# Optimization experiments

Hardware: AMD Instinct MI355X
Metric: run time of the kernel (lower is better)

Reference implementation:

```python
import jax, jax.numpy as jnp
import numpy as np

N, E, IN, HID, OUT = 100000, 1600000, 128, 128, 64


def setup_inputs() -> dict:
    key = jax.random.key(0)
    ks = jax.random.split(key, 8)
    x = jax.random.normal(ks[0], (N, IN), dtype=jnp.float32)
    edge_index = jax.random.randint(ks[1], (2, E), 0, N, dtype=jnp.int64)
    s = lambda fan_in: 1.0 / np.sqrt(fan_in)
    W1_l = jax.random.normal(ks[2], (IN, HID), dtype=jnp.float32) * s(IN)
    W1_r = jax.random.normal(ks[3], (IN, HID), dtype=jnp.float32) * s(IN)
    b1 = jnp.zeros((HID,), dtype=jnp.float32)
    W2_l = jax.random.normal(ks[4], (HID, OUT), dtype=jnp.float32) * s(HID)
    W2_r = jax.random.normal(ks[5], (HID, OUT), dtype=jnp.float32) * s(HID)
    b2 = jnp.zeros((OUT,), dtype=jnp.float32)
    return {"x": x, "edge_index": edge_index, "W1_l": W1_l, "W1_r": W1_r,
            "b1": b1, "W2_l": W2_l, "W2_r": W2_r, "b2": b2}


def sage_conv(x, src, dst, W_l, W_r, b):
    """PyG SAGEConv (aggr='mean', root_weight=True): lin_l(mean_agg) + lin_r(x)."""
    n = x.shape[0]
    msg = x[src]                                              # [E, d] gather
    agg = jax.ops.segment_sum(msg, dst, num_segments=n)       # [N, d] scatter-add
    deg = jax.ops.segment_sum(jnp.ones_like(dst, dtype=x.dtype), dst,
                              num_segments=n)                 # [N]
    mean = agg / jnp.maximum(deg, 1.0)[:, None]
    return mean @ W_l + x @ W_r + b


def reference(x, edge_index, W1_l, W1_r, b1, W2_l, W2_r, b2):
    src, dst = edge_index[0], edge_index[1]
    h = sage_conv(x, src, dst, W1_l, W1_r, b1)
    h = jax.nn.relu(h)
    # dropout(p=0.5) is identity in eval mode
    out = sage_conv(h, src, dst, W2_l, W2_r, b2)
    return out
```

## Files before the change

### kernel.cpp

```cpp
#include <hip/hip_runtime.h>

#define NN 100000
#define NE 1600000
#define PSHIFT 9
#define PSZ 512
#define NP ((NN + PSZ - 1) / PSZ)
#define BCHUNK 8192
#define NBIN ((NE + BCHUNK - 1) / BCHUNK)
#define SRCMASK 0x1FFFF

typedef __attribute__((ext_vector_type(8))) short short8;
typedef __attribute__((ext_vector_type(4))) float f32x4;

__device__ __forceinline__ ushort f2bf(float f) {
    uint u = __float_as_uint(f);
    return (ushort)((u + 0x7FFFu + ((u >> 16) & 1u)) >> 16);
}
__device__ __forceinline__ float bflo(uint u) { return __uint_as_float(u << 16); }
__device__ __forceinline__ float bfhi(uint u) { return __uint_as_float(u & 0xffff0000u); }
__device__ __forceinline__ uint packbf(float a, float b) {
    return (uint)f2bf(a) | ((uint)f2bf(b) << 16);
}

__global__ __launch_bounds__(256) void k_phist(const int* __restrict__ dst,
                                               int* __restrict__ pcnt)
{
    __shared__ int cnt[256];
    const int tid = threadIdx.x;
    cnt[tid] = 0;
    __syncthreads();
    const long e0 = (long)blockIdx.x * BCHUNK;
    for (int i = tid; i < BCHUNK; i += 256) {
        long e = e0 + i;
        if (e < NE) atomicAdd(&cnt[dst[e] >> PSHIFT], 1);
    }
    __syncthreads();
    if (cnt[tid] > 0) atomicAdd(&pcnt[tid], cnt[tid]);
}

__global__ __launch_bounds__(256) void k_pscan(const int* __restrict__ pcnt,
                                               int* __restrict__ poff,
                                               int* __restrict__ gcur,
                                               int* __restrict__ rowptr)
{
    __shared__ int tmp[256];
    const int tid = threadIdx.x;
    int v = (tid < NP) ? pcnt[tid] : 0;
    tmp[tid] = v;
    __syncthreads();
    for (int off = 1; off < 256; off <<= 1) {
        int t = (tid >= off) ? tmp[tid - off] : 0;
        __syncthreads();
        tmp[tid] += t;
        __syncthreads();
    }
    int ex = tmp[tid] - v;
    if (tid < NP) { poff[tid] = ex; gcur[tid] = ex; }
    if (tid == 0) { poff[NP] = NE; rowptr[NN] = NE; }
}

__global__ __launch_bounds__(256) void k_binning(const int* __restrict__ src,
                                                 const int* __restrict__ dst,
                                                 int* __restrict__ gcur,
                                                 uint* __restrict__ packed)
{
    __shared__ int cnt[256];
    __shared__ int base[256];
    const int tid = threadIdx.x;
    const long e0 = (long)blockIdx.x * BCHUNK;
    cnt[tid] = 0;
    __syncthreads();
    for (int i = tid; i < BCHUNK; i += 256) {
        long e = e0 + i;
        if (e < NE) atomicAdd(&cnt[dst[e] >> PSHIFT], 1);
    }
    __syncthreads();
    if (cnt[tid] > 0) base[tid] = atomicAdd(&gcur[tid], cnt[tid]);
    cnt[tid] = 0;
    __syncthreads();
    for (int i = tid; i < BCHUNK; i += 256) {
        long e = e0 + i;
        if (e < NE) {
            int d = dst[e], s = src[e];
            int p = d >> PSHIFT;
            int ofs = atomicAdd(&cnt[p], 1);
            packed[base[p] + ofs] = (uint)s | ((uint)(d & (PSZ - 1)) << 17);
        }
    }
}

__global__ __launch_bounds__(256) void k_pfill(const uint* __restrict__ packed,
                                               const int* __restrict__ poff,
                                               int* __restrict__ rowptr,
                                               int* __restrict__ col)
{
    __shared__ int cnt[PSZ];
    __shared__ int cur[PSZ];
    __shared__ int tot[256];
    const int p   = blockIdx.x;
    const int tid = threadIdx.x;
    const int beg = poff[p], end = poff[p + 1];
    cnt[tid] = 0; cnt[tid + 256] = 0;
    __syncthreads();
    for (int i = beg + tid; i < end; i += 256)
        atomicAdd(&cnt[packed[i] >> 17], 1);
    __syncthreads();
    int v0 = cnt[tid * 2], v1 = cnt[tid * 2 + 1];
    int s  = v0 + v1;
    tot[tid] = s;
    __syncthreads();
    for (int off = 1; off < 256; off <<= 1) {
        int t = (tid >= off) ? tot[tid - off] : 0;
        __syncthreads();
        tot[tid] += t;
        __syncthreads();
    }
    int ex = tot[tid] - s + beg;
    cur[tid * 2]     = ex;
    cur[tid * 2 + 1] = ex + v0;
    int n0 = p * PSZ;
    if (n0 + tid * 2     < NN) rowptr[n0 + tid * 2]     = ex;
    if (n0 + tid * 2 + 1 < NN) rowptr[n0 + tid * 2 + 1] = ex + v0;
    __syncthreads();
    for (int i = beg + tid; i < end; i += 256) {
        uint v = packed[i];
        int pos = atomicAdd(&cur[v >> 17], 1);
        col[pos] = (int)(v & SRCMASK);
    }
}

__global__ __launch_bounds__(256) void k_castw(const float* __restrict__ W1l,
                                               const float* __restrict__ W1r,
                                               const float* __restrict__ W2l,
                                               const float* __restrict__ W2r,
                                               ushort* __restrict__ WbT1,
                                               ushort* __restrict__ WbT2)
{
    int i = blockIdx.x * 256 + threadIdx.x;
    if (i < 256 * 128) {
        int c = i >> 7, k = i & 127;
        float v = (c < 128) ? W1l[k * 128 + c] : W1r[k * 128 + (c - 128)];
        WbT1[i] = f2bf(v);
    } else if (i < 256 * 128 + 128 * 128) {
        int j = i - 256 * 128;
        int c = j >> 7, k = j & 127;
        float v = (c < 64) ? W2l[k * 64 + c] : W2r[k * 64 + (c - 64)];
        WbT2[j] = f2bf(v);
    }
}

template <bool IS_L1>
__global__ __launch_bounds__(256) void k_gemmf(const void* __restrict__ Ap,
                                               const ushort* __restrict__ Bt,
                                               const float* __restrict__ bias,
                                               ushort* __restrict__ zb,
                                               void* __restrict__ yout)
{
    constexpr int CB = IS_L1 ? 4 : 2;
    constexpr int ZW = IS_L1 ? 128 : 64;
    __shared__ ushort As[64 * 128];

    const int tid = threadIdx.x, bm = blockIdx.x;

    for (int c = tid; c < 1024; c += 256) {
        int row  = c >> 4;
        int coff = (c & 15) * 8;
        int gr   = bm * 64 + row;
        short8 va;
        if (gr < NN) {
            if (IS_L1) {
                const float* A = (const float*)Ap;
                float4 f0 = *reinterpret_cast<const float4*>(A + (size_t)gr * 128 + coff);
                float4 f1 = *reinterpret_cast<const float4*>(A + (size_t)gr * 128 + coff + 4);
                va[0] = (short)f2bf(f0.x); va[1] = (short)f2bf(f0.y);
                va[2] = (short)f2bf(f0.z); va[3] = (short)f2bf(f0.w);
                va[4] = (short)f2bf(f1.x); va[5] = (short)f2bf(f1.y);
                va[6] = (short)f2bf(f1.z); va[7] = (short)f2bf(f1.w);
            } else {
                const ushort* A = (const ushort*)Ap;
                va = *reinterpret_cast<const short8*>(A + (size_t)gr * 128 + coff);
            }
        } else {
            va = short8{0, 0, 0, 0, 0, 0, 0, 0};
        }
        int byte = row * 256 + coff * 2;
        byte ^= ((row & 7) << 4);
        *reinterpret_cast<short8*>(reinterpret_cast<char*>(As) + byte) = va;
    }
    __syncthreads();

    const int wid = tid >> 6, lane = tid & 63;
    const int lr  = lane & 15;
    const int lk  = (lane >> 4) << 3;

    f32x4 acc[4][CB];
#pragma unroll
    for (int mi = 0; mi < 4; ++mi)
#pragma unroll
        for (int nf = 0; nf < CB; ++nf) acc[mi][nf] = f32x4{0.f, 0.f, 0.f, 0.f};

    const char* pA = reinterpret_cast<const char*>(As);

#pragma unroll
    for (int ks = 0; ks < 4; ++ks) {
        int k2 = (ks * 32 + lk) * 2;
        short8 a[4], b[CB];
#pragma unroll
        for (int mi = 0; mi < 4; ++mi) {
            int r = mi * 16 + lr;
            int byte = r * 256 + k2;
            byte ^= ((r & 7) << 4);
            a[mi] = *reinterpret_cast<const short8*>(pA + byte);
        }
#pragma unroll
        for (int nf = 0; nf < CB; ++nf) {
            int colB = wid * (16 * CB) + nf * 16 + lr;
            b[nf] = *reinterpret_cast<const short8*>(Bt + (size_t)colB * 128 + ks * 32 + lk);
        }
#pragma unroll
        for (int mi = 0; mi < 4; ++mi)
#pragma unroll
            for (int nf = 0; nf < CB; ++nf)
                acc[mi][nf] = __builtin_amdgcn_mfma_f32_16x16x32_bf16(a[mi], b[nf], acc[mi][nf], 0, 0, 0);
    }

#pragma unroll
    for (int mi = 0; mi < 4; ++mi) {
#pragma unroll
        for (int nf = 0; nf < CB; ++nf) {
            int colg = wid * (16 * CB) + nf * 16 + lr;
#pragma unroll
            for (int rr = 0; rr < 4; ++rr) {
                int rowg = bm * 64 + mi * 16 + ((lane >> 4) << 2) + rr;
                if (rowg < NN) {
                    float v = acc[mi][nf][rr];
                    if (colg < ZW) {
                        zb[(size_t)rowg * ZW + colg] = f2bf(v);
                    } else {
                        int c2 = colg - ZW;
                        if (IS_L1) ((ushort*)yout)[(size_t)rowg * 128 + c2] = f2bf(v + bias[c2]);
                        else       ((float*)yout)[(size_t)rowg * 64 + c2]  = v + bias[c2];
                    }
                }
            }
        }
    }
}

__global__ __launch_bounds__(256) void k_gather1(const ushort* __restrict__ z1b,
                                                 const ushort* __restrict__ y1b,
                                                 const int* __restrict__ rowptr,
                                                 const int* __restrict__ col,
                                                 ushort* __restrict__ hb)
{
    const int w = threadIdx.x >> 6, lane = threadIdx.x & 63;
    const int n = blockIdx.x * 4 + w;
    if (n >= NN) return;
    const int half = lane >> 5, li = lane & 31;
    const int beg = rowptr[n], end = rowptr[n + 1];
    const uint2* zu = (const uint2*)z1b;
    float a0 = 0.f, a1 = 0.f, a2 = 0.f, a3 = 0.f;
    int e = beg;
    for (; e + 7 < end; e += 8) {
        int s0 = col[e     + half];
        int s1 = col[e + 2 + half];
        int s2 = col[e + 4 + half];
        int s3 = col[e + 6 + half];
        uint2 u0 = zu[(size_t)s0 * 32 + li];
        uint2 u1 = zu[(size_t)s1 * 32 + li];
        uint2 u2 = zu[(size_t)s2 * 32 + li];
        uint2 u3 = zu[(size_t)s3 * 32 + li];
        a0 += bflo(u0.x) + bflo(u1.x) + bflo(u2.x) + bflo(u3.x);
        a1 += bfhi(u0.x) + bfhi(u1.x) + bfhi(u2.x) + bfhi(u3.x);
        a2 += bflo(u0.y) + bflo(u1.y) + bflo(u2.y) + bflo(u3.y);
        a3 += bfhi(u0.y) + bfhi(u1.y) + bfhi(u2.y) + bfhi(u3.y);
    }
    for (; e + 1 < end; e += 2) {
        int s0 = col[e + half];
        uint2 u0 = zu[(size_t)s0 * 32 + li];
        a0 += bflo(u0.x); a1 += bfhi(u0.x);
        a2 += bflo(u0.y); a3 += bfhi(u0.y);
    }
    if (e < end && half == 0) {
        int s0 = col[e];
        uint2 u0 = zu[(size_t)s0 * 32 + li];
        a0 += bflo(u0.x); a1 += bfhi(u0.x);
        a2 += bflo(u0.y); a3 += bfhi(u0.y);
    }
    a0 += __shfl_xor(a0, 32); a1 += __shfl_xor(a1, 32);
    a2 += __shfl_xor(a2, 32); a3 += __shfl_xor(a3, 32);
    if (half == 0) {
        float inv = 1.0f / (float)max(end - beg, 1);
        uint2 uy = ((const uint2*)y1b)[(size_t)n * 32 + li];
        float h0 = fmaxf(a0 * inv + bflo(uy.x), 0.f);
        float h1 = fmaxf(a1 * inv + bfhi(uy.x), 0.f);
        float h2 = fmaxf(a2 * inv + bflo(uy.y), 0.f);
        float h3 = fmaxf(a3 * inv + bfhi(uy.y), 0.f);
        uint2 o;
        o.x = packbf(h0, h1);
        o.y = packbf(h2, h3);
        ((uint2*)hb)[(size_t)n * 32 + li] = o;
    }
}

__global__ __launch_bounds__(256) void k_gather2(const ushort* __restrict__ z2b,
                                                 const float* __restrict__ y2f,
                                                 const int* __restrict__ rowptr,
                                                 const int* __restrict__ col,
                                                 float* __restrict__ out)
{
    const int w = threadIdx.x >> 6, lane = threadIdx.x & 63;
    const int n = blockIdx.x * 4 + w;
    if (n >= NN) return;
    const int quar = lane >> 4, li = lane & 15;
    const int beg = rowptr[n], end = rowptr[n + 1];
    const uint2* zu = (const uint2*)z2b;
    float a0 = 0.f, a1 = 0.f, a2 = 0.f, a3 = 0.f;
    int e = beg;
    for (; e + 15 < end; e += 16) {
        int s0 = col[e      + quar];
        int s1 = col[e + 4  + quar];
        int s2 = col[e + 8  + quar];
        int s3 = col[e + 12 + quar];
        uint2 u0 = zu[(size_t)s0 * 16 + li];
        uint2 u1 = zu[(size_t)s1 * 16 + li];
        uint2 u2 = zu[(size_t)s2 * 16 + li];
        uint2 u3 = zu[(size_t)s3 * 16 + li];
        a0 += bflo(u0.x) + bflo(u1.x) + bflo(u2.x) + bflo(u3.x);
        a1 += bfhi(u0.x) + bfhi(u1.x) + bfhi(u2.x) + bfhi(u3.x);
        a2 += bflo(u0.y) + bflo(u1.y) + bflo(u2.y) + bflo(u3.y);
        a3 += bfhi(u0.y) + bfhi(u1.y) + bfhi(u2.y) + bfhi(u3.y);
    }
    for (; e + 3 < end; e += 4) {
        int s0 = col[e + quar];
        uint2 u0 = zu[(size_t)s0 * 16 + li];
        a0 += bflo(u0.x); a1 += bfhi(u0.x);
        a2 += bflo(u0.y); a3 += bfhi(u0.y);
    }
    int rem = end - e;
    if (quar < rem) {
        int s0 = col[e + quar];
        uint2 u0 = zu[(size_t)s0 * 16 + li];
        a0 += bflo(u0.x); a1 += bfhi(u0.x);
        a2 += bflo(u0.y); a3 += bfhi(u0.y);
    }
    a0 += __shfl_xor(a0, 16); a1 += __shfl_xor(a1, 16);
    a2 += __shfl_xor(a2, 16); a3 += __shfl_xor(a3, 16);
    a0 += __shfl_xor(a0, 32); a1 += __shfl_xor(a1, 32);
    a2 += __shfl_xor(a2, 32); a3 += __shfl_xor(a3, 32);
    if (quar == 0) {
        float inv = 1.0f / (float)max(end - beg, 1);
        float4 y = ((const float4*)y2f)[(size_t)n * 16 + li];
        float4 o;
        o.x = a0 * inv + y.x;
        o.y = a1 * inv + y.y;
        o.z = a2 * inv + y.z;
        o.w = a3 * inv + y.w;
        ((float4*)out)[(size_t)n * 16 + li] = o;
    }
}

extern "C" void kernel_launch(void* const* d_in, const int* in_sizes, int n_in,
                              void* d_out, int out_size, void* d_ws, size_t ws_size,
                              hipStream_t stream)
{
    const float* x   = (const float*)d_in[0];
    const int*   ei  = (const int*)d_in[1];
    const float* W1l = (const float*)d_in[2];
    const float* W1r = (const float*)d_in[3];
    const float* b1  = (const float*)d_in[4];
    const float* W2l = (const float*)d_in[5];
    const float* W2r = (const float*)d_in[6];
    const float* b2  = (const float*)d_in[7];
    float* out = (float*)d_out;

    const int* src = ei;
    const int* dst = ei + NE;

    int*  rowptr = (int*)d_ws;
    int*  pcnt   = rowptr + NN + 1;
    int*  poff   = pcnt + 256;
    int*  gcur   = poff + 256;
    uint* packed = (uint*)(gcur + 256);
    int*  colA   = (int*)(packed + NE);
    uintptr_t p = (uintptr_t)(colA + NE);
    p = (p + 255) & ~(uintptr_t)255;
    ushort* WbT1 = (ushort*)p;  p += (size_t)256 * 128 * 2;
    ushort* WbT2 = (ushort*)p;  p += (size_t)128 * 128 * 2;
    p = (p + 255) & ~(uintptr_t)255;
    ushort* z1b = (ushort*)p;   p += (size_t)NN * 128 * 2;
    ushort* y1b = (ushort*)p;   p += (size_t)NN * 128 * 2;
    ushort* hb  = (ushort*)p;   p += (size_t)NN * 128 * 2;
    ushort* z2b = z1b;
    float*  y2f = (float*)y1b;

    hipMemsetAsync(pcnt, 0, 256 * sizeof(int), stream);
    k_phist<<<NBIN, 256, 0, stream>>>(dst, pcnt);
    k_pscan<<<1, 256, 0, stream>>>(pcnt, poff, gcur, rowptr);
    k_binning<<<NBIN, 256, 0, stream>>>(src, dst, gcur, packed);
    k_pfill<<<NP, 256, 0, stream>>>(packed, poff, rowptr, colA);

    k_castw<<<(256 * 128 + 128 * 128 + 255) / 256, 256, 0, stream>>>(
        W1l, W1r, W2l, W2r, WbT1, WbT2);

    const int GM = (NN + 63) / 64;

    k_gemmf<true><<<GM, 256, 0, stream>>>(x, WbT1, b1, z1b, y1b);
    k_gather1<<<(NN + 3) / 4, 256, 0, stream>>>(z1b, y1b, rowptr, colA, hb);

    k_gemmf<false><<<GM, 256, 0, stream>>>(hb, WbT2, b2, z2b, y2f);
    k_gather2<<<(NN + 3) / 4, 256, 0, stream>>>(z2b, y2f, rowptr, colA, out);
}
```

Measured before the change: 276.6 us.

## Make GEMM persistent with register-resident B and double-buffered A tiles

Replaces the one-tile-per-block GEMM with a persistent kernel of 512 blocks and 512 threads that keeps the B fragments in registers and loops over row tiles. Each A tile is prefetched into registers while the current one is computed from a double-buffered LDS. The fp32-to-bf16 cast of x moves into a separate pre-pass kernel. This removes repeated B loads and per-block startup, and overlaps global A loads with MFMA work. The cost is an extra kernel launch plus a full write and re-read of a bf16 copy of x.

```diff
diff --git a/kernel.cpp b/kernel.cpp
--- a/kernel.cpp
+++ b/kernel.cpp
@@ -8,6 +8,8 @@
 #define BCHUNK 8192
 #define NBIN ((NE + BCHUNK - 1) / BCHUNK)
 #define SRCMASK 0x1FFFF
+#define GMTILES ((NN + 63) / 64)
+#define GEMM_GB 512
 
 typedef __attribute__((ext_vector_type(8))) short short8;
 typedef __attribute__((ext_vector_type(4))) float f32x4;
@@ -149,101 +151,125 @@
     }
 }
 
-template <bool IS_L1>
-__global__ __launch_bounds__(256) void k_gemmf(const void* __restrict__ Ap,
-                                               const ushort* __restrict__ Bt,
-                                               const float* __restrict__ bias,
-                                               ushort* __restrict__ zb,
-                                               void* __restrict__ yout)
-{
-    constexpr int CB = IS_L1 ? 4 : 2;
-    constexpr int ZW = IS_L1 ? 128 : 64;
-    __shared__ ushort As[64 * 128];
-
-    const int tid = threadIdx.x, bm = blockIdx.x;
-
-    for (int c = tid; c < 1024; c += 256) {
-        int row  = c >> 4;
-        int coff = (c & 15) * 8;
-        int gr   = bm * 64 + row;
-        short8 va;
-        if (gr < NN) {
-            if (IS_L1) {
-                const float* A = (const float*)Ap;
-                float4 f0 = *reinterpret_cast<const float4*>(A + (size_t)gr * 128 + coff);
-                float4 f1 = *reinterpret_cast<const float4*>(A + (size_t)gr * 128 + coff + 4);
-                va[0] = (short)f2bf(f0.x); va[1] = (short)f2bf(f0.y);
-                va[2] = (short)f2bf(f0.z); va[3] = (short)f2bf(f0.w);
-                va[4] = (short)f2bf(f1.x); va[5] = (short)f2bf(f1.y);
-                va[6] = (short)f2bf(f1.z); va[7] = (short)f2bf(f1.w);
-            } else {
-                const ushort* A = (const ushort*)Ap;
-                va = *reinterpret_cast<const short8*>(A + (size_t)gr * 128 + coff);
-            }
-        } else {
-            va = short8{0, 0, 0, 0, 0, 0, 0, 0};
-        }
-        int byte = row * 256 + coff * 2;
-        byte ^= ((row & 7) << 4);
-        *reinterpret_cast<short8*>(reinterpret_cast<char*>(As) + byte) = va;
-    }
-    __syncthreads();
-
-    const int wid = tid >> 6, lane = tid & 63;
-    const int lr  = lane & 15;
-    const int lk  = (lane >> 4) << 3;
-
-    f32x4 acc[4][CB];
-#pragma unroll
-    for (int mi = 0; mi < 4; ++mi)
-#pragma unroll
-        for (int nf = 0; nf < CB; ++nf) acc[mi][nf] = f32x4{0.f, 0.f, 0.f, 0.f};
-
-    const char* pA = reinterpret_cast<const char*>(As);
-
-#pragma unroll
-    for (int ks = 0; ks < 4; ++ks) {
-        int k2 = (ks * 32 + lk) * 2;
-        short8 a[4], b[CB];
-#pragma unroll
-        for (int mi = 0; mi < 4; ++mi) {
-            int r = mi * 16 + lr;
-            int byte = r * 256 + k2;
-            byte ^= ((r & 7) << 4);
-            a[mi] = *reinterpret_cast<const short8*>(pA + byte);
-        }
+__global__ __launch_bounds__(256) void k_castx(const float* __restrict__ x,
+                                               ushort* __restrict__ xb)
+{
+    const int CH = NN * 16;
+    for (int i = blockIdx.x * 256 + threadIdx.x; i < CH; i += 256 * 2048) {
+        float4 f0 = ((const float4*)x)[(size_t)i * 2];
+        float4 f1 = ((const float4*)x)[(size_t)i * 2 + 1];
+        short8 v;
+        v[0] = (short)f2bf(f0.x); v[1] = (short)f2bf(f0.y);
+        v[2] = (short)f2bf(f0.z); v[3] = (short)f2bf(f0.w);
+        v[4] = (short)f2bf(f1.x); v[5] = (short)f2bf(f1.y);
+        v[6] = (short)f2bf(f1.z); v[7] = (short)f2bf(f1.w);
+        ((short8*)xb)[i] = v;
+    }
+}
+
+template <int CB, int NCOL, bool YF32>
+__global__ __launch_bounds__(512) void k_gemm(const ushort* __restrict__ Ab,
+                                              const ushort* __restrict__ Bt,
+                                              const float* __restrict__ bias,
+                                              ushort* __restrict__ zb,
+                                              void* __restrict__ yout)
+{
+    constexpr int ZW = NCOL / 2;
+    __shared__ ushort As[2][64 * 128];
+
+    const int tid  = threadIdx.x;
+    const int wid  = tid >> 6, lane = tid & 63;
+    const int lr   = lane & 15;
+    const int lk   = (lane >> 4) << 3;
+
+    short8 bfr[4][CB];
+#pragma unroll
+    for (int ks = 0; ks < 4; ++ks)
 #pragma unroll
         for (int nf = 0; nf < CB; ++nf) {
             int colB = wid * (16 * CB) + nf * 16 + lr;
-            b[nf] = *reinterpret_cast<const short8*>(Bt + (size_t)colB * 128 + ks * 32 + lk);
+            bfr[ks][nf] = *reinterpret_cast<const short8*>(
+                Bt + (size_t)colB * 128 + ks * 32 + lk);
         }
+
+    const int p0 = tid * 16, p1 = p0 + 8192;
+    const int r0 = p0 >> 8, r1 = p1 >> 8;
+    const int d0 = p0 ^ ((r0 & 7) << 4);
+    const int d1 = p1 ^ ((r1 & 7) << 4);
+    const int e0 = (p0 & 255) >> 1;
+    const int e1 = (p1 & 255) >> 1;
+
+    const short8 zero8 = {0, 0, 0, 0, 0, 0, 0, 0};
+    short8 sA0, sA1;
+
+    int t = blockIdx.x;
+    {
+        int gr0 = t * 64 + r0, gr1 = t * 64 + r1;
+        sA0 = (gr0 < NN) ? *reinterpret_cast<const short8*>(Ab + (size_t)gr0 * 128 + e0) : zero8;
+        sA1 = (gr1 < NN) ? *reinterpret_cast<const short8*>(Ab + (size_t)gr1 * 128 + e1) : zero8;
+    }
+
+    int cur = 0;
+    for (; t < GMTILES; t += GEMM_GB) {
+        char* wbase = reinterpret_cast<char*>(As[cur]);
+        *reinterpret_cast<short8*>(wbase + d0) = sA0;
+        *reinterpret_cast<short8*>(wbase + d1) = sA1;
+        __syncthreads();
+
+        int tn = t + GEMM_GB;
+        if (tn < GMTILES) {
+            int gr0 = tn * 64 + r0, gr1 = tn * 64 + r1;
+            sA0 = (gr0 < NN) ? *reinterpret_cast<const short8*>(Ab + (size_t)gr0 * 128 + e0) : zero8;
+            sA1 = (gr1 < NN) ? *reinterpret_cast<const short8*>(Ab + (size_t)gr1 * 128 + e1) : zero8;
+        }
+
+        f32x4 acc[4][CB];
 #pragma unroll
         for (int mi = 0; mi < 4; ++mi)
 #pragma unroll
-            for (int nf = 0; nf < CB; ++nf)
-                acc[mi][nf] = __builtin_amdgcn_mfma_f32_16x16x32_bf16(a[mi], b[nf], acc[mi][nf], 0, 0, 0);
-    }
-
-#pragma unroll
-    for (int mi = 0; mi < 4; ++mi) {
-#pragma unroll
-        for (int nf = 0; nf < CB; ++nf) {
-            int colg = wid * (16 * CB) + nf * 16 + lr;
-#pragma unroll
-            for (int rr = 0; rr < 4; ++rr) {
-                int rowg = bm * 64 + mi * 16 + ((lane >> 4) << 2) + rr;
-                if (rowg < NN) {
-                    float v = acc[mi][nf][rr];
-                    if (colg < ZW) {
-                        zb[(size_t)rowg * ZW + colg] = f2bf(v);
-                    } else {
-                        int c2 = colg - ZW;
-                        if (IS_L1) ((ushort*)yout)[(size_t)rowg * 128 + c2] = f2bf(v + bias[c2]);
-                        else       ((float*)yout)[(size_t)rowg * 64 + c2]  = v + bias[c2];
+            for (int nf = 0; nf < CB; ++nf) acc[mi][nf] = f32x4{0.f, 0.f, 0.f, 0.f};
+
+        const char* pA = reinterpret_cast<const char*>(As[cur]);
+#pragma unroll
+        for (int ks = 0; ks < 4; ++ks) {
+            int k2 = (ks * 32 + lk) * 2;
+            short8 a[4];
+#pragma unroll
+            for (int mi = 0; mi < 4; ++mi) {
+                int r = mi * 16 + lr;
+                int byte = (r * 256 + k2) ^ ((r & 7) << 4);
+                a[mi] = *reinterpret_cast<const short8*>(pA + byte);
+            }
+#pragma unroll
+            for (int mi = 0; mi < 4; ++mi)
+#pragma unroll
+                for (int nf = 0; nf < CB; ++nf)
+                    acc[mi][nf] = __builtin_amdgcn_mfma_f32_16x16x32_bf16(
+                        a[mi], bfr[ks][nf], acc[mi][nf], 0, 0, 0);
+        }
+
+#pragma unroll
+        for (int mi = 0; mi < 4; ++mi) {
+#pragma unroll
+            for (int nf = 0; nf < CB; ++nf) {
+                int colg = wid * (16 * CB) + nf * 16 + lr;
+#pragma unroll
+                for (int rr = 0; rr < 4; ++rr) {
+                    int rowg = t * 64 + mi * 16 + ((lane >> 4) << 2) + rr;
+                    if (rowg < NN) {
+                        float v = acc[mi][nf][rr];
+                        if (colg < ZW) {
+                            zb[(size_t)rowg * ZW + colg] = f2bf(v);
+                        } else {
+                            int c2 = colg - ZW;
+                            if (YF32) ((float*)yout)[(size_t)rowg * ZW + c2]  = v + bias[c2];
+                            else      ((ushort*)yout)[(size_t)rowg * ZW + c2] = f2bf(v + bias[c2]);
+                        }
                     }
                 }
             }
         }
+        cur ^= 1;
     }
 }
 
@@ -388,6 +414,7 @@
     ushort* WbT1 = (ushort*)p;  p += (size_t)256 * 128 * 2;
     ushort* WbT2 = (ushort*)p;  p += (size_t)128 * 128 * 2;
     p = (p + 255) & ~(uintptr_t)255;
+    ushort* xb  = (ushort*)p;   p += (size_t)NN * 128 * 2;
     ushort* z1b = (ushort*)p;   p += (size_t)NN * 128 * 2;
     ushort* y1b = (ushort*)p;   p += (size_t)NN * 128 * 2;
     ushort* hb  = (ushort*)p;   p += (size_t)NN * 128 * 2;
@@ -402,12 +429,11 @@
 
     k_castw<<<(256 * 128 + 128 * 128 + 255) / 256, 256, 0, stream>>>(
         W1l, W1r, W2l, W2r, WbT1, WbT2);
-
-    const int GM = (NN + 63) / 64;
-
-    k_gemmf<true><<<GM, 256, 0, stream>>>(x, WbT1, b1, z1b, y1b);
+    k_castx<<<2048, 256, 0, stream>>>(x, xb);
+
+    k_gemm<2, 256, false><<<GEMM_GB, 512, 0, stream>>>(xb, WbT1, b1, z1b, y1b);
     k_gather1<<<(NN + 3) / 4, 256, 0, stream>>>(z1b, y1b, rowptr, colA, hb);
 
-    k_gemmf<false><<<GM, 256, 0, stream>>>(hb, WbT2, b2, z2b, y2f);
+    k_gemm<1, 128, true><<<GEMM_GB, 512, 0, stream>>>(hb, WbT2, b2, z2b, y2f);
     k_gather2<<<(NN + 3) / 4, 256, 0, stream>>>(z2b, y2f, rowptr, colA, out);
 }
```

Measured after the change: 268.0 us. 1.03x faster.
